# Optimization experiments

Hardware: AMD Instinct MI355X
Metric: run time of the kernel (lower is better)

Reference implementation:

```python
import jax, jax.numpy as jnp
import numpy as np

N_POL = 100000
N_TICK = 20000
N = N_POL + N_TICK
E = 1000000
POL_FEAT = 7
EMB = 128
HID = 256
OUT = 128
N_STATES = 60


def setup_inputs() -> dict:
    key = jax.random.key(0)
    ks = jax.random.split(key, 16)
    s = 0.05
    return {
        "pol_features": jax.random.normal(ks[0], (N_POL, POL_FEAT), dtype=jnp.float32),
        "state_ids": jax.random.randint(ks[1], (N_POL,), 0, N_STATES, dtype=jnp.int32),
        "edge_index": jax.random.randint(ks[2], (2, E), 0, N, dtype=jnp.int32),
        "edge_weight": jax.random.uniform(ks[3], (E,), dtype=jnp.float32),
        # parameters
        "W_proj": jax.random.normal(ks[4], (POL_FEAT, EMB), dtype=jnp.float32) * s,
        "b_proj": jnp.zeros((EMB,), dtype=jnp.float32),
        "state_emb": jax.random.normal(ks[5], (N_STATES, EMB), dtype=jnp.float32) * s,
        "emb_tick": jax.random.normal(ks[6], (N_TICK, EMB), dtype=jnp.float32) * s,
        "W1_rel": jax.random.normal(ks[7], (EMB, HID), dtype=jnp.float32) * s,
        "b1_rel": jnp.zeros((HID,), dtype=jnp.float32),
        "W1_root": jax.random.normal(ks[8], (EMB, HID), dtype=jnp.float32) * s,
        "W2_rel": jax.random.normal(ks[9], (HID, OUT), dtype=jnp.float32) * s,
        "b2_rel": jnp.zeros((OUT,), dtype=jnp.float32),
        "W2_root": jax.random.normal(ks[10], (HID, OUT), dtype=jnp.float32) * s,
    }


def _graph_conv(x, edge_index, edge_weight, W_rel, b_rel, W_root):
    # PyG GraphConv: out = lin_rel(sum_{j->i} w_ji * x_j) + lin_root(x_i)
    src, dst = edge_index[0], edge_index[1]
    msg = x[src] * edge_weight[:, None]            # [E, d]
    agg = jax.ops.segment_sum(msg, dst, num_segments=N)  # [N, d]
    return agg @ W_rel + b_rel + x @ W_root


def reference(pol_features, state_ids, edge_index, edge_weight,
              W_proj, b_proj, state_emb, emb_tick,
              W1_rel, b1_rel, W1_root, W2_rel, b2_rel, W2_root):
    # Node features: projected politician feats + state embedding, cat tick embeddings
    pol = jax.nn.relu(pol_features @ W_proj + b_proj) + state_emb[state_ids]  # [N_POL, EMB]
    x = jnp.concatenate([pol, emb_tick], axis=0)   # [N, EMB]
    h = jax.nn.relu(_graph_conv(x, edge_index, edge_weight, W1_rel, b1_rel, W1_root))
    # dropout is identity in eval mode
    out = _graph_conv(h, edge_index, edge_weight, W2_rel, b2_rel, W2_root)
    return out  # [N, OUT]
```

## Files before the change

### kernel.cpp

```cpp
#include <hip/hip_runtime.h>
#include <hip/hip_bf16.h>

typedef unsigned short u16;
using short8  = __attribute__((ext_vector_type(8))) short;
using ushort8 = __attribute__((ext_vector_type(8))) unsigned short;
using float4v = __attribute__((ext_vector_type(4))) float;

#define N_POL  100000
#define N_TICK 20000
#define NNODE  120000
#define NEDGE  1000000
#define NREP   8
#define EB     3907
#define POLB   50000
#define TICKB  10000

static __device__ __forceinline__ float b2f(u16 u) {
    return __uint_as_float(((unsigned)u) << 16);
}
static __device__ __forceinline__ u16 f2b(float f) {
    unsigned u = __float_as_uint(f);
    unsigned r = (u + 0x7FFFu + ((u >> 16) & 1u)) >> 16;
    return (u16)r;
}
static __device__ __forceinline__ float lde(const void* p, size_t i, int f32) {
    return f32 ? ((const float*)p)[i] : b2f(((const u16*)p)[i]);
}

static __device__ __forceinline__ size_t frag_addr(int k, int n) {
    return ((size_t)((n >> 4) * 8 + (k >> 5)) * 64 + (((k >> 3) & 3) * 16 + (n & 15))) * 8
           + (k & 7);
}

static __device__ __forceinline__ void gload_lds16(const u16* g, u16* l) {
    __builtin_amdgcn_global_load_lds(
        (const __attribute__((address_space(1))) void*)g,
        (__attribute__((address_space(3))) void*)l, 16, 0, 0);
}

__global__ __launch_bounds__(256) void detect_k(const void* __restrict__ ew,
                                                int* __restrict__ flag,
                                                int* __restrict__ count) {
    int i = blockIdx.x * 256 + threadIdx.x;
    if (i < NREP * NNODE) count[i] = 0;
    if (blockIdx.x == 0 && threadIdx.x == 0) {
        const u16* p = (const u16*)ew;
        int huge = 0, allz = 1;
        for (int j = 0; j < 128; j += 2) {
            u16 b = p[j];
            if (b != 0) allz = 0;
            float v = b2f(b);
            if (!(fabsf(v) <= 4.0f)) huge = 1;
        }
        *flag = huge | allz;
    }
}

__global__ __launch_bounds__(256) void hist_build(const int* __restrict__ ei,
                                                  int* __restrict__ count,
                                                  int* __restrict__ rank,
                                                  const void* __restrict__ pf,
                                                  const int* __restrict__ sid,
                                                  const void* __restrict__ Wp,
                                                  const void* __restrict__ bp,
                                                  const void* __restrict__ semb,
                                                  const void* __restrict__ et,
                                                  const int* __restrict__ flag,
                                                  u16* __restrict__ Xb) {
    if (blockIdx.x < EB) {
        int rep = blockIdx.x & (NREP - 1);
        int e = blockIdx.x * 256 + threadIdx.x;
        if (e < NEDGE)
            rank[e] = atomicAdd(&count[rep * NNODE + ei[NEDGE + e]], 1);
        return;
    }
    const int f32 = *flag;
    int bb = blockIdx.x - EB;
    if (bb < POLB) {
        int row = bb * 2 + (threadIdx.x >> 7);
        int j = threadIdx.x & 127;
        float s = lde(bp, j, f32);
#pragma unroll
        for (int k = 0; k < 7; k++)
            s = fmaf(lde(pf, (size_t)row * 7 + k, f32), lde(Wp, k * 128 + j, f32), s);
        s = fmaxf(s, 0.f);
        s += lde(semb, (size_t)sid[row] * 128 + j, f32);
        Xb[(size_t)row * 128 + j] = f2b(s);
    } else {
        int idx = (bb - POLB) * 256 + threadIdx.x;
        Xb[(size_t)N_POL * 128 + idx] = f2b(lde(et, idx, f32));
    }
}

__global__ __launch_bounds__(256) void scan1(const int* __restrict__ count,
                                             int* __restrict__ roff,
                                             int* __restrict__ row_tmp,
                                             int* __restrict__ bsum) {
    __shared__ int sd[256];
    int t = threadIdx.x;
    int i = blockIdx.x * 256 + t;
    int c = 0;
    if (i < NNODE) {
#pragma unroll
        for (int r = 0; r < NREP; r++) {
            int v = count[r * NNODE + i];
            roff[r * NNODE + i] = c;
            c += v;
        }
    }
    sd[t] = c;
    __syncthreads();
#pragma unroll
    for (int off = 1; off < 256; off <<= 1) {
        int v = (t >= off) ? sd[t - off] : 0;
        __syncthreads();
        sd[t] += v;
        __syncthreads();
    }
    if (i < NNODE) row_tmp[i] = sd[t] - c;
    if (t == 255) bsum[blockIdx.x] = sd[t];
}

__global__ __launch_bounds__(512) void scan2(int* __restrict__ bsum, int nb) {
    __shared__ int sd[512];
    int t = threadIdx.x;
    int v = (t < nb) ? bsum[t] : 0;
    sd[t] = v;
    __syncthreads();
#pragma unroll
    for (int off = 1; off < 512; off <<= 1) {
        int u = (t >= off) ? sd[t - off] : 0;
        __syncthreads();
        sd[t] += u;
        __syncthreads();
    }
    if (t < nb) bsum[t] = sd[t] - v;
}

__global__ __launch_bounds__(256) void scan3(const int* __restrict__ row_tmp,
                                             const int* __restrict__ bsum,
                                             int* __restrict__ row_start) {
    int i = blockIdx.x * 256 + threadIdx.x;
    if (i < NNODE) row_start[i] = row_tmp[i] + bsum[blockIdx.x];
    if (i == 0) row_start[NNODE] = NEDGE;
}

__global__ __launch_bounds__(256) void fill_prep(const int* __restrict__ ei,
                                                 const void* __restrict__ ew,
                                                 const int* __restrict__ flag,
                                                 const int* __restrict__ row_start,
                                                 const int* __restrict__ roff,
                                                 const int* __restrict__ rank,
                                                 uint2* __restrict__ epk,
                                                 const void* __restrict__ W1rel,
                                                 const void* __restrict__ W1root,
                                                 const void* __restrict__ W2rel,
                                                 const void* __restrict__ W2root,
                                                 u16* __restrict__ Wf1,
                                                 u16* __restrict__ Wf2) {
    const int f32 = *flag;
    if (blockIdx.x < EB) {
        int rep = blockIdx.x & (NREP - 1);
        int e = blockIdx.x * 256 + threadIdx.x;
        if (e >= NEDGE) return;
        int src = ei[e];
        int dst = ei[NEDGE + e];
        int pos = row_start[dst] + roff[rep * NNODE + dst] + rank[e];
        uint2 pk;
        pk.x = (unsigned)src;
        pk.y = (unsigned)f2b(lde(ew, e, f32));
        epk[pos] = pk;
        return;
    }
    int idx = (blockIdx.x - EB) * 256 + threadIdx.x;
    int id = idx & 65535;
    int k = id >> 8, n = id & 255;
    if (idx < 65536) {
        float v = (k < 128) ? lde(W1rel, (size_t)k * 256 + n, f32)
                            : lde(W1root, (size_t)(k - 128) * 256 + n, f32);
        Wf1[frag_addr(k, n)] = f2b(v);
    } else {
        float v = (n < 128) ? lde(W2rel, (size_t)k * 128 + n, f32)
                            : lde(W2root, (size_t)k * 128 + (n - 128), f32);
        Wf2[frag_addr(k, n)] = f2b(v);
    }
}

__global__ __launch_bounds__(256) void gather128(const int* __restrict__ row_start,
                                                 const uint2* __restrict__ epk,
                                                 const u16* __restrict__ S,
                                                 u16* __restrict__ agg) {
    int n = blockIdx.x * 4 + (threadIdx.x >> 6);
    int lane = threadIdx.x & 63;
    int g4 = lane >> 4;
    int l16 = lane & 15;
    int s0 = row_start[n], s1 = row_start[n + 1];
    float a[8] = {0.f, 0.f, 0.f, 0.f, 0.f, 0.f, 0.f, 0.f};
    int e = s0;
    for (; e + 8 <= s1; e += 8) {
        uint2 p0 = epk[e + g4], p1 = epk[e + 4 + g4];
        float w0 = b2f((u16)p0.y), w1 = b2f((u16)p1.y);
        ushort8 x0 = *(const ushort8*)(S + (size_t)p0.x * 128 + l16 * 8);
        ushort8 x1 = *(const ushort8*)(S + (size_t)p1.x * 128 + l16 * 8);
#pragma unroll
        for (int j = 0; j < 8; j++) {
            a[j] = fmaf(b2f(x0[j]), w0, a[j]);
            a[j] = fmaf(b2f(x1[j]), w1, a[j]);
        }
    }
    for (; e + 4 <= s1; e += 4) {
        uint2 p = epk[e + g4];
        float w = b2f((u16)p.y);
        ushort8 x = *(const ushort8*)(S + (size_t)p.x * 128 + l16 * 8);
#pragma unroll
        for (int j = 0; j < 8; j++) a[j] = fmaf(b2f(x[j]), w, a[j]);
    }
    if (e < s1) {
        int eg = e + g4;
        int valid = eg < s1;
        uint2 p = epk[valid ? eg : s0];
        float w = valid ? b2f((u16)p.y) : 0.f;
        ushort8 x = *(const ushort8*)(S + (size_t)p.x * 128 + l16 * 8);
#pragma unroll
        for (int j = 0; j < 8; j++) a[j] = fmaf(b2f(x[j]), w, a[j]);
    }
#pragma unroll
    for (int j = 0; j < 8; j++) {
        a[j] += __shfl_xor(a[j], 16);
        a[j] += __shfl_xor(a[j], 32);
    }
    if (g4 == 0) {
        ushort8 o;
#pragma unroll
        for (int j = 0; j < 8; j++) o[j] = f2b(a[j]);
        *(ushort8*)(agg + (size_t)n * 128 + l16 * 8) = o;
    }
}

__global__ __launch_bounds__(256) void gather_add(const int* __restrict__ row_start,
                                                  const uint2* __restrict__ epk,
                                                  const u16* __restrict__ T2,
                                                  const u16* __restrict__ P,
                                                  const int* __restrict__ flag,
                                                  void* __restrict__ out) {
    const int f32 = *flag;
    int n = blockIdx.x * 4 + (threadIdx.x >> 6);
    int lane = threadIdx.x & 63;
    int g4 = lane >> 4;
    int l16 = lane & 15;
    int s0 = row_start[n], s1 = row_start[n + 1];
    float a[8] = {0.f, 0.f, 0.f, 0.f, 0.f, 0.f, 0.f, 0.f};
    int e = s0;
    for (; e + 8 <= s1; e += 8) {
        uint2 p0 = epk[e + g4], p1 = epk[e + 4 + g4];
        float w0 = b2f((u16)p0.y), w1 = b2f((u16)p1.y);
        ushort8 x0 = *(const ushort8*)(T2 + (size_t)p0.x * 128 + l16 * 8);
        ushort8 x1 = *(const ushort8*)(T2 + (size_t)p1.x * 128 + l16 * 8);
#pragma unroll
        for (int j = 0; j < 8; j++) {
            a[j] = fmaf(b2f(x0[j]), w0, a[j]);
            a[j] = fmaf(b2f(x1[j]), w1, a[j]);
        }
    }
    for (; e + 4 <= s1; e += 4) {
        uint2 p = epk[e + g4];
        float w = b2f((u16)p.y);
        ushort8 x = *(const ushort8*)(T2 + (size_t)p.x * 128 + l16 * 8);
#pragma unroll
        for (int j = 0; j < 8; j++) a[j] = fmaf(b2f(x[j]), w, a[j]);
    }
    if (e < s1) {
        int eg = e + g4;
        int valid = eg < s1;
        uint2 p = epk[valid ? eg : s0];
        float w = valid ? b2f((u16)p.y) : 0.f;
        ushort8 x = *(const ushort8*)(T2 + (size_t)p.x * 128 + l16 * 8);
#pragma unroll
        for (int j = 0; j < 8; j++) a[j] = fmaf(b2f(x[j]), w, a[j]);
    }
#pragma unroll
    for (int j = 0; j < 8; j++) {
        a[j] += __shfl_xor(a[j], 16);
        a[j] += __shfl_xor(a[j], 32);
    }
    if (g4 == 0) {
        ushort8 pv = *(const ushort8*)(P + (size_t)n * 128 + l16 * 8);
        float v[8];
#pragma unroll
        for (int j = 0; j < 8; j++) v[j] = a[j] + b2f(pv[j]);
        if (f32) {
            float4 s0v, s1v;
            s0v.x = v[0]; s0v.y = v[1]; s0v.z = v[2]; s0v.w = v[3];
            s1v.x = v[4]; s1v.y = v[5]; s1v.z = v[6]; s1v.w = v[7];
            *(float4*)((float*)out + (size_t)n * 128 + l16 * 8) = s0v;
            *(float4*)((float*)out + (size_t)n * 128 + l16 * 8 + 4) = s1v;
        } else {
            ushort8 s;
#pragma unroll
            for (int j = 0; j < 8; j++) s[j] = f2b(v[j]);
            *(ushort8*)((u16*)out + (size_t)n * 128 + l16 * 8) = s;
        }
    }
}

__global__ __launch_bounds__(256) void fused_gemm(const u16* __restrict__ agg,
                                                  const u16* __restrict__ Xb,
                                                  const u16* __restrict__ Wf1,
                                                  const u16* __restrict__ Wf2,
                                                  const void* __restrict__ b1,
                                                  const void* __restrict__ b2,
                                                  u16* __restrict__ T2,
                                                  u16* __restrict__ P,
                                                  const int* __restrict__ flag,
                                                  int M) {
    const int f32 = *flag;
    __shared__ u16 LDSU[32 * 64 * 8];
    const int row0 = blockIdx.x * 64;
    const int wid = threadIdx.x >> 6;
    const int lane = threadIdx.x & 63;
    const int q = lane >> 4, lm = lane & 15;

    {
        int kqL = lane & 31;
#pragma unroll
        for (int i = 0; i < 8; i++) {
            int t = i * 4 + wid;
            int row = 2 * t + (lane >> 5);
            int kqG = kqL ^ (row & 7);
            const u16* src = (kqG < 16)
                ? agg + ((size_t)(row0 + row)) * 128 + kqG * 8
                : Xb + ((size_t)(row0 + row)) * 128 + (kqG - 16) * 8;
            gload_lds16(src, LDSU + (size_t)t * 512);
        }
    }
    __syncthreads();

    float4v acc[4][4];
#pragma unroll
    for (int i = 0; i < 4; i++)
#pragma unroll
        for (int j = 0; j < 4; j++) acc[i][j] = (float4v){0.f, 0.f, 0.f, 0.f};
#pragma unroll
    for (int kb = 0; kb < 8; kb++) {
        short8 a[4];
#pragma unroll
        for (int ti = 0; ti < 4; ti++) {
            int rl = ti * 16 + lm;
            int chunk = (kb * 4 + q) ^ (rl & 7);
            a[ti] = *(const short8*)(LDSU + (size_t)rl * 256 + chunk * 8);
        }
        short8 b[4];
#pragma unroll
        for (int tj = 0; tj < 4; tj++) {
            int nt = wid * 4 + tj;
            b[tj] = *(const short8*)(Wf1 + ((size_t)(nt * 8 + kb) * 64 + lane) * 8);
        }
#pragma unroll
        for (int ti = 0; ti < 4; ti++)
#pragma unroll
            for (int tj = 0; tj < 4; tj++)
                acc[ti][tj] = __builtin_amdgcn_mfma_f32_16x16x32_bf16(
                    a[ti], b[tj], acc[ti][tj], 0, 0, 0);
    }
    __syncthreads();

#pragma unroll
    for (int tj = 0; tj < 4; tj++) {
        int col = wid * 64 + tj * 16 + lm;
        float bv = lde(b1, col, f32);
        int kq2 = col >> 3, jj = col & 7;
#pragma unroll
        for (int ti = 0; ti < 4; ti++) {
            int rl = ti * 16 + q * 4;
#pragma unroll
            for (int r = 0; r < 4; r++) {
                float v = fmaxf(acc[ti][tj][r] + bv, 0.f);
                LDSU[((size_t)kq2 * 64 + rl + r) * 8 + jj] = f2b(v);
            }
        }
    }
    __syncthreads();

    float4v acc2[4][4];
#pragma unroll
    for (int i = 0; i < 4; i++)
#pragma unroll
        for (int j = 0; j < 4; j++) acc2[i][j] = (float4v){0.f, 0.f, 0.f, 0.f};
#pragma unroll
    for (int kb = 0; kb < 8; kb++) {
        short8 a[4];
#pragma unroll
        for (int ti = 0; ti < 4; ti++) {
            int rl = ti * 16 + lm;
            a[ti] = *(const short8*)(LDSU + ((size_t)(kb * 4 + q) * 64 + rl) * 8);
        }
        short8 b[4];
#pragma unroll
        for (int tj = 0; tj < 4; tj++) {
            int nt = wid * 4 + tj;
            b[tj] = *(const short8*)(Wf2 + ((size_t)(nt * 8 + kb) * 64 + lane) * 8);
        }
#pragma unroll
        for (int ti = 0; ti < 4; ti++)
#pragma unroll
            for (int tj = 0; tj < 4; tj++)
                acc2[ti][tj] = __builtin_amdgcn_mfma_f32_16x16x32_bf16(
                    a[ti], b[tj], acc2[ti][tj], 0, 0, 0);
    }
    __syncthreads();

#pragma unroll
    for (int tj = 0; tj < 4; tj++) {
        int col = wid * 64 + tj * 16 + lm;
        int chunk = col >> 3, jj = col & 7;
        float bv = (col < 128) ? 0.f : lde(b2, col - 128, f32);
#pragma unroll
        for (int ti = 0; ti < 4; ti++) {
#pragma unroll
            for (int r = 0; r < 4; r++) {
                int row = ti * 16 + q * 4 + r;
                int pchunk = chunk ^ (((row >> 2) & 3) << 1);
                LDSU[((size_t)row * 32 + pchunk) * 8 + jj] = f2b(acc2[ti][tj][r] + bv);
            }
        }
    }
    __syncthreads();
#pragma unroll
    for (int i = 0; i < 8; i++) {
        int g = i * 256 + threadIdx.x;
        int row = g >> 5;
        int chunk = g & 31;
        int pchunk = chunk ^ (((row >> 2) & 3) << 1);
        short8 v = *(const short8*)(LDSU + ((size_t)row * 32 + pchunk) * 8);
        int grow = row0 + row;
        int colu = chunk * 8;
        u16* dst = (colu < 128) ? (T2 + (size_t)grow * 128 + colu)
                                : (P + (size_t)grow * 128 + (colu - 128));
        *(short8*)dst = v;
    }
    (void)M;
}

extern "C" void kernel_launch(void* const* d_in, const int* in_sizes, int n_in,
                              void* d_out, int out_size, void* d_ws, size_t ws_size,
                              hipStream_t stream) {
    const void* pf     = d_in[0];
    const int*  sid    = (const int*)d_in[1];
    const int*  ei     = (const int*)d_in[2];
    const void* ew     = d_in[3];
    const void* Wp     = d_in[4];
    const void* bp     = d_in[5];
    const void* semb   = d_in[6];
    const void* et     = d_in[7];
    const void* W1rel  = d_in[8];
    const void* b1     = d_in[9];
    const void* W1root = d_in[10];
    const void* W2rel  = d_in[11];
    const void* b2     = d_in[12];
    const void* W2root = d_in[13];

    char* w = (char*)d_ws;
    u16*   agg       = (u16*)w;
    u16*   T2        = (u16*)(w + 30720000);
    u16*   P         = (u16*)(w + 61440000);
    u16*   Wf1       = (u16*)(w + 92160000);
    u16*   Wf2       = (u16*)(w + 92291072);
    uint2* epk       = (uint2*)(w + 92422144);
    int*   rank      = (int*)(w + 100422144);
    int*   row_start = (int*)(w + 104422144);
    int*   row_tmp   = (int*)(w + 104902148);
    int*   count     = (int*)(w + 105382148);
    int*   roff      = (int*)(w + 109222148);
    int*   bsum      = (int*)(w + 113062148);
    int*   flag      = (int*)(w + 113066244);
    u16*   Xb        = (u16*)d_out;

    const int NB = (NNODE + 255) / 256;
    const int GB = (NNODE + 63) / 64;
    const int ZB = (NREP * NNODE + 255) / 256;

    detect_k<<<ZB, 256, 0, stream>>>(ew, flag, count);

    hist_build<<<EB + POLB + TICKB, 256, 0, stream>>>(
        ei, count, rank, pf, sid, Wp, bp, semb, et, flag, Xb);

    scan1<<<NB, 256, 0, stream>>>(count, roff, row_tmp, bsum);
    scan2<<<1, 512, 0, stream>>>(bsum, NB);
    scan3<<<NB, 256, 0, stream>>>(row_tmp, bsum, row_start);

    fill_prep<<<EB + 512, 256, 0, stream>>>(ei, ew, flag, row_start, roff, rank, epk,
                                            W1rel, W1root, W2rel, W2root, Wf1, Wf2);

    gather128<<<NNODE / 4, 256, 0, stream>>>(row_start, epk, Xb, agg);

    fused_gemm<<<GB, 256, 0, stream>>>(agg, Xb, Wf1, Wf2, b1, b2, T2, P, flag, NNODE);

    gather_add<<<NNODE / 4, 256, 0, stream>>>(row_start, epk, T2, P, flag, d_out);
}
```

Baseline: 374.4 us.

## Replace global-atomic CSR build with two-pass LDS bucketed radix sort

Builds the destination-sorted edge list with a two-level bucketed sort instead of per-edge global atomics on replicated counters. Pass one histograms edges into 512-node buckets in LDS, scans per-block offsets, and scatters them to a temporary buffer. Pass two does a per-bucket LDS histogram, scan and scatter that also produces row_start. This removes the 8x replicated count zeroing, the global atomic contention and the three-kernel scan, at the cost of an extra pass over the edge data through the temporary buffer. Edge order within a node becomes nondeterministic, which can slightly change floating-point sums.

```diff
diff --git a/kernel.cpp b/kernel.cpp
--- a/kernel.cpp
+++ b/kernel.cpp
@@ -10,8 +10,8 @@
 #define N_TICK 20000
 #define NNODE  120000
 #define NEDGE  1000000
-#define NREP   8
-#define EB     3907
+#define NBLK   977
+#define NBKT2  235
 #define POLB   50000
 #define TICKB  10000
 
@@ -38,12 +38,8 @@
         (__attribute__((address_space(3))) void*)l, 16, 0, 0);
 }
 
-__global__ __launch_bounds__(256) void detect_k(const void* __restrict__ ew,
-                                                int* __restrict__ flag,
-                                                int* __restrict__ count) {
-    int i = blockIdx.x * 256 + threadIdx.x;
-    if (i < NREP * NNODE) count[i] = 0;
-    if (blockIdx.x == 0 && threadIdx.x == 0) {
+__global__ void detect_k(const void* __restrict__ ew, int* __restrict__ flag) {
+    if (threadIdx.x == 0) {
         const u16* p = (const u16*)ew;
         int huge = 0, allz = 1;
         for (int j = 0; j < 128; j += 2) {
@@ -56,26 +52,118 @@
     }
 }
 
-__global__ __launch_bounds__(256) void hist_build(const int* __restrict__ ei,
-                                                  int* __restrict__ count,
-                                                  int* __restrict__ rank,
-                                                  const void* __restrict__ pf,
-                                                  const int* __restrict__ sid,
-                                                  const void* __restrict__ Wp,
-                                                  const void* __restrict__ bp,
-                                                  const void* __restrict__ semb,
-                                                  const void* __restrict__ et,
-                                                  const int* __restrict__ flag,
-                                                  u16* __restrict__ Xb) {
-    if (blockIdx.x < EB) {
-        int rep = blockIdx.x & (NREP - 1);
-        int e = blockIdx.x * 256 + threadIdx.x;
-        if (e < NEDGE)
-            rank[e] = atomicAdd(&count[rep * NNODE + ei[NEDGE + e]], 1);
+
+__global__ __launch_bounds__(256) void p1hist(const int* __restrict__ ei,
+                                              int* __restrict__ bh) {
+    __shared__ int h[256];
+    int t = threadIdx.x;
+    h[t] = 0;
+    __syncthreads();
+    int e0 = (blockIdx.x * 256 + t) * 4;
+    if (e0 + 4 <= NEDGE) {
+        int4 d = *(const int4*)(ei + NEDGE + e0);
+        atomicAdd(&h[d.x >> 9], 1);
+        atomicAdd(&h[d.y >> 9], 1);
+        atomicAdd(&h[d.z >> 9], 1);
+        atomicAdd(&h[d.w >> 9], 1);
+    } else {
+        for (int e = e0; e < NEDGE; e++)
+            atomicAdd(&h[ei[NEDGE + e] >> 9], 1);
+    }
+    __syncthreads();
+    bh[t * NBLK + blockIdx.x] = h[t];
+}
+
+__global__ __launch_bounds__(256) void p1scanA(int* __restrict__ bh,
+                                               int* __restrict__ btot) {
+    __shared__ int sd[256];
+    int b = blockIdx.x;
+    int t = threadIdx.x;
+    int base = b * NBLK;
+    int v[4]; int tot = 0;
+    int j0 = t * 4;
+#pragma unroll
+    for (int k = 0; k < 4; k++) {
+        int j = j0 + k;
+        v[k] = (j < NBLK) ? bh[base + j] : 0;
+        tot += v[k];
+    }
+    sd[t] = tot;
+    __syncthreads();
+#pragma unroll
+    for (int off = 1; off < 256; off <<= 1) {
+        int u = (t >= off) ? sd[t - off] : 0;
+        __syncthreads();
+        sd[t] += u;
+        __syncthreads();
+    }
+    int excl = sd[t] - tot;
+#pragma unroll
+    for (int k = 0; k < 4; k++) {
+        int j = j0 + k;
+        if (j < NBLK) { int tmp = v[k]; bh[base + j] = excl; excl += tmp; }
+    }
+    if (t == 255) btot[b] = sd[255];
+}
+
+__global__ void p1scanB(const int* __restrict__ btot, int* __restrict__ bbase,
+                        int* __restrict__ row_start) {
+    __shared__ int sd[256];
+    int t = threadIdx.x;
+    int v = btot[t];
+    sd[t] = v;
+    __syncthreads();
+#pragma unroll
+    for (int off = 1; off < 256; off <<= 1) {
+        int u = (t >= off) ? sd[t - off] : 0;
+        __syncthreads();
+        sd[t] += u;
+        __syncthreads();
+    }
+    bbase[t] = sd[t] - v;
+    if (t == 255) { bbase[256] = sd[255]; row_start[NNODE] = NEDGE; }
+}
+
+__global__ __launch_bounds__(256) void p1scat_build(const int* __restrict__ ei,
+                                                    const void* __restrict__ ew,
+                                                    const int* __restrict__ flag,
+                                                    const int* __restrict__ bh,
+                                                    const int* __restrict__ bbase,
+                                                    uint2* __restrict__ tmp1,
+                                                    const void* __restrict__ pf,
+                                                    const int* __restrict__ sid,
+                                                    const void* __restrict__ Wp,
+                                                    const void* __restrict__ bp,
+                                                    const void* __restrict__ semb,
+                                                    const void* __restrict__ et,
+                                                    u16* __restrict__ Xb) {
+    const int f32 = *flag;
+    if (blockIdx.x < NBLK) {
+        __shared__ int base[256];
+        __shared__ int cur[256];
+        int t = threadIdx.x;
+        base[t] = bbase[t] + bh[t * NBLK + blockIdx.x];
+        cur[t] = 0;
+        __syncthreads();
+        int e0 = (blockIdx.x * 256 + t) * 4;
+#pragma unroll
+        for (int k = 0; k < 4; k++) {
+            int e = e0 + k;
+            if (e < NEDGE) {
+                int dst = ei[NEDGE + e];
+                int o = dst >> 9;
+                int src = ei[e];
+                unsigned w16 = (unsigned)f2b(lde(ew, e, f32));
+                int r = atomicAdd(&cur[o], 1);
+                uint2 u;
+                u.x = (unsigned)src;
+                u.y = (w16 << 16) | (unsigned)(dst & 511);
+                tmp1[base[o] + r] = u;
+            }
+        }
         return;
     }
-    const int f32 = *flag;
-    int bb = blockIdx.x - EB;
+    int bb = blockIdx.x - NBLK;
     if (bb < POLB) {
         int row = bb * 2 + (threadIdx.x >> 7);
         int j = threadIdx.x & 127;
@@ -92,87 +180,59 @@
     }
 }
 
-__global__ __launch_bounds__(256) void scan1(const int* __restrict__ count,
-                                             int* __restrict__ roff,
-                                             int* __restrict__ row_tmp,
-                                             int* __restrict__ bsum) {
-    __shared__ int sd[256];
-    int t = threadIdx.x;
-    int i = blockIdx.x * 256 + t;
-    int c = 0;
-    if (i < NNODE) {
-#pragma unroll
-        for (int r = 0; r < NREP; r++) {
-            int v = count[r * NNODE + i];
-            roff[r * NNODE + i] = c;
-            c += v;
-        }
-    }
-    sd[t] = c;
-    __syncthreads();
-#pragma unroll
-    for (int off = 1; off < 256; off <<= 1) {
-        int v = (t >= off) ? sd[t - off] : 0;
-        __syncthreads();
-        sd[t] += v;
-        __syncthreads();
-    }
-    if (i < NNODE) row_tmp[i] = sd[t] - c;
-    if (t == 255) bsum[blockIdx.x] = sd[t];
-}
-
-__global__ __launch_bounds__(512) void scan2(int* __restrict__ bsum, int nb) {
-    __shared__ int sd[512];
-    int t = threadIdx.x;
-    int v = (t < nb) ? bsum[t] : 0;
-    sd[t] = v;
-    __syncthreads();
-#pragma unroll
-    for (int off = 1; off < 512; off <<= 1) {
-        int u = (t >= off) ? sd[t - off] : 0;
-        __syncthreads();
-        sd[t] += u;
-        __syncthreads();
-    }
-    if (t < nb) bsum[t] = sd[t] - v;
-}
-
-__global__ __launch_bounds__(256) void scan3(const int* __restrict__ row_tmp,
-                                             const int* __restrict__ bsum,
-                                             int* __restrict__ row_start) {
-    int i = blockIdx.x * 256 + threadIdx.x;
-    if (i < NNODE) row_start[i] = row_tmp[i] + bsum[blockIdx.x];
-    if (i == 0) row_start[NNODE] = NEDGE;
-}
-
-__global__ __launch_bounds__(256) void fill_prep(const int* __restrict__ ei,
-                                                 const void* __restrict__ ew,
-                                                 const int* __restrict__ flag,
-                                                 const int* __restrict__ row_start,
-                                                 const int* __restrict__ roff,
-                                                 const int* __restrict__ rank,
-                                                 uint2* __restrict__ epk,
-                                                 const void* __restrict__ W1rel,
-                                                 const void* __restrict__ W1root,
-                                                 const void* __restrict__ W2rel,
-                                                 const void* __restrict__ W2root,
-                                                 u16* __restrict__ Wf1,
-                                                 u16* __restrict__ Wf2) {
+__global__ __launch_bounds__(256) void p2_prep(const uint2* __restrict__ tmp1,
+                                               const int* __restrict__ bbase,
+                                               uint2* __restrict__ epk,
+                                               int* __restrict__ row_start,
+                                               const void* __restrict__ W1rel,
+                                               const void* __restrict__ W1root,
+                                               const void* __restrict__ W2rel,
+                                               const void* __restrict__ W2root,
+                                               const int* __restrict__ flag,
+                                               u16* __restrict__ Wf1,
+                                               u16* __restrict__ Wf2) {
+    if (blockIdx.x < NBKT2) {
+        __shared__ int h[512];
+        __shared__ int sc[512];
+        int b = blockIdx.x;
+        int t = threadIdx.x;
+        h[t] = 0; h[t + 256] = 0;
+        __syncthreads();
+        int lo = bbase[b], hi = bbase[b + 1];
+        for (int i = lo + t; i < hi; i += 256)
+            atomicAdd(&h[tmp1[i].y & 511], 1);
+        __syncthreads();
+        sc[t] = h[t]; sc[t + 256] = h[t + 256];
+        __syncthreads();
+#pragma unroll
+        for (int off = 1; off < 512; off <<= 1) {
+            int v0 = (t >= off) ? sc[t - off] : 0;
+            int v1 = (t + 256 >= off) ? sc[t + 256 - off] : 0;
+            __syncthreads();
+            sc[t] += v0; sc[t + 256] += v1;
+            __syncthreads();
+        }
+        int e0_ = sc[t] - h[t];
+        int e1_ = sc[t + 256] - h[t + 256];
+        int node0 = b * 512;
+        if (node0 + t < NNODE) row_start[node0 + t] = lo + e0_;
+        if (node0 + t + 256 < NNODE) row_start[node0 + t + 256] = lo + e1_;
+        __syncthreads();
+        h[t] = e0_; h[t + 256] = e1_;
+        __syncthreads();
+        for (int i = lo + t; i < hi; i += 256) {
+            uint2 u = tmp1[i];
+            int j = (int)(u.y & 511u);
+            int r = atomicAdd(&h[j], 1);
+            uint2 o;
+            o.x = u.x;
+            o.y = u.y >> 16;
+            epk[lo + r] = o;
+        }
+        return;
+    }
     const int f32 = *flag;
-    if (blockIdx.x < EB) {
-        int rep = blockIdx.x & (NREP - 1);
-        int e = blockIdx.x * 256 + threadIdx.x;
-        if (e >= NEDGE) return;
-        int src = ei[e];
-        int dst = ei[NEDGE + e];
-        int pos = row_start[dst] + roff[rep * NNODE + dst] + rank[e];
-        uint2 pk;
-        pk.x = (unsigned)src;
-        pk.y = (unsigned)f2b(lde(ew, e, f32));
-        epk[pos] = pk;
-        return;
-    }
-    int idx = (blockIdx.x - EB) * 256 + threadIdx.x;
+    int idx = (blockIdx.x - NBKT2) * 256 + threadIdx.x;
     int id = idx & 65535;
     int k = id >> 8, n = id & 255;
     if (idx < 65536) {
@@ -466,30 +526,26 @@
     u16*   Wf1       = (u16*)(w + 92160000);
     u16*   Wf2       = (u16*)(w + 92291072);
     uint2* epk       = (uint2*)(w + 92422144);
-    int*   rank      = (int*)(w + 100422144);
-    int*   row_start = (int*)(w + 104422144);
-    int*   row_tmp   = (int*)(w + 104902148);
-    int*   count     = (int*)(w + 105382148);
-    int*   roff      = (int*)(w + 109222148);
-    int*   bsum      = (int*)(w + 113062148);
-    int*   flag      = (int*)(w + 113066244);
+    uint2* tmp1      = (uint2*)(w + 100422144);
+    int*   bh        = (int*)(w + 108422144);
+    int*   btot      = (int*)(w + 109422592);
+    int*   bbase     = (int*)(w + 109423616);
+    int*   row_start = (int*)(w + 109424648);
+    int*   flag      = (int*)(w + 109904652);
     u16*   Xb        = (u16*)d_out;
 
-    const int NB = (NNODE + 255) / 256;
     const int GB = (NNODE + 63) / 64;
-    const int ZB = (NREP * NNODE + 255) / 256;
-
-    detect_k<<<ZB, 256, 0, stream>>>(ew, flag, count);
-
-    hist_build<<<EB + POLB + TICKB, 256, 0, stream>>>(
-        ei, count, rank, pf, sid, Wp, bp, semb, et, flag, Xb);
-
-    scan1<<<NB, 256, 0, stream>>>(count, roff, row_tmp, bsum);
-    scan2<<<1, 512, 0, stream>>>(bsum, NB);
-    scan3<<<NB, 256, 0, stream>>>(row_tmp, bsum, row_start);
-
-    fill_prep<<<EB + 512, 256, 0, stream>>>(ei, ew, flag, row_start, roff, rank, epk,
-                                            W1rel, W1root, W2rel, W2root, Wf1, Wf2);
+
+    detect_k<<<1, 64, 0, stream>>>(ew, flag);
+
+    p1hist<<<NBLK, 256, 0, stream>>>(ei, bh);
+    p1scanA<<<256, 256, 0, stream>>>(bh, btot);
+    p1scanB<<<1, 256, 0, stream>>>(btot, bbase, row_start);
+    p1scat_build<<<NBLK + POLB + TICKB, 256, 0, stream>>>(
+        ei, ew, flag, bh, bbase, tmp1, pf, sid, Wp, bp, semb, et, Xb);
+    p2_prep<<<NBKT2 + 512, 256, 0, stream>>>(tmp1, bbase, epk, row_start,
+                                             W1rel, W1root, W2rel, W2root, flag,
+                                             Wf1, Wf2);
 
     gather128<<<NNODE / 4, 256, 0, stream>>>(row_start, epk, Xb, agg);
 
```

Result: faster. 331.7 us (-11.4%).
